# Kernel tuning notes

Hardware: AMD Instinct MI355X
Metric: run time of the kernel (lower is better)

Reference implementation:

```python
import jax, jax.numpy as jnp
import numpy as np

EPS = 1e-5


def conv3x3(x, w):
    # x: [B,C,H,W], w: [O,I,3,3], stride 1, pad 1 (torch Conv2d bias=False)
    return jax.lax.conv_general_dilated(
        x, w, window_strides=(1, 1), padding=((1, 1), (1, 1)),
        dimension_numbers=("NCHW", "OIHW", "NCHW"))


def batchnorm(y, g, b, m, v):
    # inference-style BN with running stats
    s = (g * jax.lax.rsqrt(v + EPS)).reshape(1, -1, 1, 1)
    t = (b - m * g * jax.lax.rsqrt(v + EPS)).reshape(1, -1, 1, 1)
    return y * s + t


def setup_inputs() -> dict:
    key = jax.random.key(0)
    ks = jax.random.split(key, 12)
    bs, c, h, w, T = 32, 64, 96, 96, 64
    inp = {}
    inp["x"] = jax.random.normal(ks[0], (bs, c, h, w), jnp.float32)
    inp["ref_x"] = jax.random.normal(ks[1], (bs, c, 1, 1), jnp.float32)
    inp["ref_types"] = jax.random.randint(ks[2], (bs,), 0, T, jnp.int32)
    # feat_extract: two BasicConv2d (conv3x3 no bias + BN + ReLU)
    inp["conv1_w"] = jax.random.normal(ks[3], (c, c, 3, 3), jnp.float32) * 0.05
    inp["bn1_g"] = jnp.ones((c,), jnp.float32)
    inp["bn1_b"] = jnp.zeros((c,), jnp.float32)
    inp["bn1_m"] = jnp.zeros((c,), jnp.float32)
    inp["bn1_v"] = jnp.ones((c,), jnp.float32)
    inp["conv2_w"] = jax.random.normal(ks[4], (c, c, 3, 3), jnp.float32) * 0.05
    inp["bn2_g"] = jnp.ones((c,), jnp.float32)
    inp["bn2_b"] = jnp.zeros((c,), jnp.float32)
    inp["bn2_m"] = jnp.zeros((c,), jnp.float32)
    inp["bn2_v"] = jnp.ones((c,), jnp.float32)
    # weight_mlp: Linear(c, 2c) -> ReLU -> Linear(2c, T)
    inp["mlp_w1"] = jax.random.normal(ks[5], (c, 2 * c), jnp.float32) * 0.05
    inp["mlp_b1"] = jnp.zeros((2 * c,), jnp.float32)
    inp["mlp_w2"] = jax.random.normal(ks[6], (2 * c, T), jnp.float32) * 0.05
    inp["mlp_b2"] = jnp.zeros((T,), jnp.float32)
    # reference buffer (torch registers zeros; use small randn so output is nontrivial)
    inp["ref_proj"] = jax.random.normal(ks[7], (T, c), jnp.float32) * 0.05
    return inp


def reference(x, ref_x, ref_types, conv1_w, bn1_g, bn1_b, bn1_m, bn1_v,
              conv2_w, bn2_g, bn2_b, bn2_m, bn2_v,
              mlp_w1, mlp_b1, mlp_w2, mlp_b2, ref_proj):
    momentum = jnp.float32(0.99)
    temperature = jnp.float32(1.0)
    bs, c, h, w = x.shape
    T = ref_proj.shape[0]

    # feat_extract + global average pool
    f = jax.nn.relu(batchnorm(conv3x3(x, conv1_w), bn1_g, bn1_b, bn1_m, bn1_v))
    f = jax.nn.relu(batchnorm(conv3x3(f, conv2_w), bn2_g, bn2_b, bn2_m, bn2_v))
    x_feat = f.mean(axis=(2, 3))  # [bs, c]

    # weight MLP -> tempered softmax
    type_logits = jax.nn.relu(x_feat @ mlp_w1 + mlp_b1) @ mlp_w2 + mlp_b2  # [bs, T]
    type_weights = jax.nn.softmax(type_logits / temperature, axis=1)

    # sequential per-sample EMA scatter, vectorized in closed form:
    # ref_new[t] = m^{k_t} * ref_proj[t] + sum_i 1[type_i=t] (1-m) m^{#later occ of t} v_i
    ref_vec = ref_x.reshape(bs, c)
    onehot = jax.nn.one_hot(ref_types, T, dtype=x.dtype)        # [bs, T]
    counts = onehot.sum(axis=0)                                  # [T]
    occ_after = counts[None, :] - jnp.cumsum(onehot, axis=0)     # strictly-after count
    w_i = (1.0 - momentum) * (momentum ** occ_after) * onehot    # [bs, T]
    ref_new = (momentum ** counts)[:, None] * ref_proj + w_i.T @ ref_vec  # [T, c]

    # weighted reference from (updated) buffer
    weighted_ref = (type_weights @ ref_new).reshape(bs, c, 1, 1)
    out = weighted_ref + ref_x

    # supervision loss: cross entropy (mean)
    logp = jax.nn.log_softmax(type_logits, axis=1)
    loss = -jnp.take_along_axis(logp, ref_types[:, None].astype(jnp.int32), axis=1).mean()
    return out, loss, ref_new
```

## Files before the change

kernel.cpp:

```cpp
#include <hip/hip_runtime.h>
#include <math.h>

#define BATCH 32
#define CH    64
#define HH    96
#define WW    96
#define NT    64

using short8 = __attribute__((ext_vector_type(8))) short;
using f32x16 = __attribute__((ext_vector_type(16))) float;

#define WS_XFS   0
#define WS_ZERO  8192
#define WS_A1    8448
#define WS_A2    82176
#define WS_XT    155904
#define WS_F1T   37904640
#define PLANE    9437184

__device__ __forceinline__ unsigned short b16(float f) {
    unsigned int u = __builtin_bit_cast(unsigned int, f);
    unsigned int r = (u + 0x7FFFu + ((u >> 16) & 1u)) >> 16;
    return (unsigned short)r;
}

__device__ __forceinline__ void gl_lds16(const void* g, void* l) {
    __builtin_amdgcn_global_load_lds(
        (const __attribute__((address_space(1))) unsigned int*)g,
        (__attribute__((address_space(3))) unsigned int*)l, 16, 0, 0);
}

__global__ void prep_small(const float* __restrict__ c1w, const float* __restrict__ c2w,
                           char* __restrict__ ws) {
    const int bid = blockIdx.x, tx = threadIdx.x;
    if (bid < 288) {
        const float* w = bid < 144 ? c1w : c2w;
        unsigned short* At = (unsigned short*)(ws + (bid < 144 ? WS_A1 : WS_A2));
        int idx = (bid % 144) * 256 + tx;
        int j = idx & 7, g1 = idx >> 3;
        int ga = g1 % 576, mc = g1 / 576;
        int c = mc & 3, mt = mc >> 2;
        int tap = ga >> 6, kb = (ga >> 5) & 1, ol = ga & 31;
        int o = mt * 32 + ol, ci = c * 16 + kb * 8 + j;
        At[idx] = b16(w[(o * 64 + ci) * 9 + tap]);
    } else {
        int i = (bid - 288) * 256 + tx;
        if (i < 2112) ((float*)ws)[i] = 0.f;
    }
}

__global__ __launch_bounds__(256)
void prep_x(const float* __restrict__ x, char* __restrict__ xt) {
    int gid = blockIdx.x * 256 + threadIdx.x;
    int cig = gid / 147456;
    int pp  = gid % 147456;
    int p   = pp * 2;
    int b   = p / 9216;
    int hw  = p % 9216;
    const float* src = x + (size_t)(b * 64 + cig * 8) * 9216 + hw;
    float2 v0 = *(const float2*)(src + 0 * 9216);
    float2 v1 = *(const float2*)(src + 1 * 9216);
    float2 v2 = *(const float2*)(src + 2 * 9216);
    float2 v3 = *(const float2*)(src + 3 * 9216);
    float2 v4 = *(const float2*)(src + 4 * 9216);
    float2 v5 = *(const float2*)(src + 5 * 9216);
    float2 v6 = *(const float2*)(src + 6 * 9216);
    float2 v7 = *(const float2*)(src + 7 * 9216);
    int c = cig >> 1, kb2 = cig & 1;
    char* dst = xt + (size_t)c * PLANE + (size_t)p * 32 + kb2 * 16;
    ushort4 a0, a1, c0, c1;
    a0.x = b16(v0.x); a0.y = b16(v1.x); a0.z = b16(v2.x); a0.w = b16(v3.x);
    a1.x = b16(v4.x); a1.y = b16(v5.x); a1.z = b16(v6.x); a1.w = b16(v7.x);
    c0.x = b16(v0.y); c0.y = b16(v1.y); c0.z = b16(v2.y); c0.w = b16(v3.y);
    c1.x = b16(v4.y); c1.y = b16(v5.y); c1.z = b16(v6.y); c1.w = b16(v7.y);
    *(ushort4*)(dst)      = a0; *(ushort4*)(dst + 8)  = a1;
    *(ushort4*)(dst + 32) = c0; *(ushort4*)(dst + 40) = c1;
}

template <int POOL>
__global__ __launch_bounds__(512, 2)
void conv_mfma(const char* __restrict__ xt, const char* __restrict__ Aprep,
               const char* __restrict__ zerop,
               const float* __restrict__ gg, const float* __restrict__ bb,
               const float* __restrict__ mm, const float* __restrict__ vv_,
               char* __restrict__ f1t, float* __restrict__ xfs) {
    __shared__ char smem[31232];
    float* s_s = (float*)(smem + 30720);
    float* s_t = s_s + 64;

    const int tx = threadIdx.x;
    const int r0 = blockIdx.x * 8;
    const int b  = blockIdx.y;
    const int wv = tx >> 6, l = tx & 63;
    const int rh = wv;
    const int kb = l >> 5, ln = l & 31;

    if (tx < 64) {
        float inv = rsqrtf(vv_[tx] + 1e-5f);
        s_s[tx] = gg[tx] * inv;
        s_t[tx] = bb[tx] - mm[tx] * gg[tx] * inv;
    }

    const char* sin[4];
    bool oob[4];
#pragma unroll
    for (int i = 0; i < 4; ++i) {
        int q = wv + 8 * i;
        int g = q * 64 + l;
        int row = g / 192, t = g % 192;
        int kb2 = t / 96, col = t % 96;
        int grow = r0 - 1 + row;
        oob[i] = (grow < 0) || (grow >= 96);
        int gr = oob[i] ? 0 : grow;
        sin[i] = xt + (size_t)((b * 96 + gr) * 96 + col) * 32 + kb2 * 16;
    }
    const char* abase = Aprep + (kb * 32 + ln) * 16;

    int bcol[3][3];
#pragma unroll
    for (int nt = 0; nt < 3; ++nt)
#pragma unroll
        for (int dw = 0; dw < 3; ++dw) {
            int cc = nt * 32 + ln + dw - 1;
            int ccc = cc < 0 ? 0 : (cc > 95 ? 95 : cc);
            bcol[nt][dw] = kb * 1536 + ccc * 16;
        }
    const bool msk0 = (ln == 0), msk2 = (ln == 31);

    f32x16 acc[2][3] = {};

#pragma unroll
    for (int c = 0; c < 4; ++c) {
        __syncthreads();
#pragma unroll
        for (int i = 0; i < 4; ++i) {
            int q = wv + 8 * i;
            if (q < 30) {
                const char* s = oob[i] ? zerop : (sin[i] + (size_t)c * PLANE);
                gl_lds16(s, smem + q * 1024);
            }
        }
        short8 af[2][9];
#pragma unroll
        for (int mt = 0; mt < 2; ++mt)
#pragma unroll
            for (int tap = 0; tap < 9; ++tap)
                af[mt][tap] = *(const short8*)(abase + mt * 36864 + c * 9216 + tap * 1024);
        __syncthreads();

        const char* brow = smem + rh * 3072;
#pragma unroll
        for (int tap = 0; tap < 9; ++tap) {
            const int dh = tap / 3, dw = tap % 3;
#pragma unroll
            for (int nt = 0; nt < 3; ++nt) {
                short8 bf = *(const short8*)(brow + dh * 3072 + bcol[nt][dw]);
                if (nt == 0 && dw == 0) bf = msk0 ? (short8){} : bf;
                if (nt == 2 && dw == 2) bf = msk2 ? (short8){} : bf;
                acc[0][nt] = __builtin_amdgcn_mfma_f32_32x32x16_bf16(af[0][tap], bf, acc[0][nt], 0, 0, 0);
                acc[1][nt] = __builtin_amdgcn_mfma_f32_32x32x16_bf16(af[1][tap], bf, acc[1][nt], 0, 0, 0);
            }
        }
    }

    const int r = r0 + rh;
    if (POOL == 0) {
#pragma unroll
        for (int nt = 0; nt < 3; ++nt) {
            int p = (b * 96 + r) * 96 + nt * 32 + ln;
            char* pb = f1t + (size_t)p * 32 + kb * 8;
#pragma unroll
            for (int mt = 0; mt < 2; ++mt)
#pragma unroll
                for (int qh = 0; qh < 4; ++qh) {
                    const int ob = mt * 32 + 8 * qh + 4 * kb;
                    float y0 = fmaxf(fmaf(acc[mt][nt][qh * 4 + 0], s_s[ob + 0], s_t[ob + 0]), 0.f);
                    float y1 = fmaxf(fmaf(acc[mt][nt][qh * 4 + 1], s_s[ob + 1], s_t[ob + 1]), 0.f);
                    float y2 = fmaxf(fmaf(acc[mt][nt][qh * 4 + 2], s_s[ob + 2], s_t[ob + 2]), 0.f);
                    float y3 = fmaxf(fmaf(acc[mt][nt][qh * 4 + 3], s_s[ob + 3], s_t[ob + 3]), 0.f);
                    uint2 pk;
                    pk.x = (unsigned)b16(y0) | ((unsigned)b16(y1) << 16);
                    pk.y = (unsigned)b16(y2) | ((unsigned)b16(y3) << 16);
                    *(uint2*)(pb + (size_t)(mt * 2 + (qh >> 1)) * PLANE + (qh & 1) * 16) = pk;
                }
        }
    } else {
#pragma unroll
        for (int mt = 0; mt < 2; ++mt)
#pragma unroll
            for (int qh = 0; qh < 4; ++qh)
#pragma unroll
                for (int j = 0; j < 4; ++j) {
                    const int o = mt * 32 + 8 * qh + 4 * kb + j;
                    const float ss = s_s[o], tt = s_t[o];
                    float y = fmaxf(fmaf(acc[mt][0][qh * 4 + j], ss, tt), 0.f)
                            + fmaxf(fmaf(acc[mt][1][qh * 4 + j], ss, tt), 0.f)
                            + fmaxf(fmaf(acc[mt][2][qh * 4 + j], ss, tt), 0.f);
#pragma unroll
                    for (int off = 1; off < 32; off <<= 1) y += __shfl_xor(y, off, 64);
                    if (ln == 0) atomicAdd(&xfs[b * 64 + o], y);
                }
    }
}

__global__ __launch_bounds__(1024)
void head_kernel(const float* __restrict__ xfs, const float* __restrict__ rx,
                 const int* __restrict__ ty_g,
                 const float* __restrict__ w1, const float* __restrict__ b1,
                 const float* __restrict__ w2, const float* __restrict__ b2,
                 const float* __restrict__ rproj, float* __restrict__ out) {
    __shared__ float xf[BATCH][64];
    __shared__ float hb[BATCH][128];
    __shared__ float lg[BATCH][NT];
    __shared__ float rnew[NT][64];
    __shared__ float rxs[BATCH * 64];
    __shared__ int   ty[BATCH];
    __shared__ float lossb[BATCH];

    const int tx = threadIdx.x;

    for (int i = tx; i < BATCH * 64; i += 1024) {
        xf[i >> 6][i & 63] = xfs[i] * (1.f / 9216.f);
        rxs[i] = rx[i];
    }
    if (tx < BATCH) ty[tx] = ty_g[tx];
    __syncthreads();

    {
        int idx = tx;
#pragma unroll
        for (int u = 0; u < 4; ++u, idx += 1024) {
            int bb_ = idx >> 7, j = idx & 127;
            float s = b1[j];
#pragma unroll 8
            for (int c = 0; c < 64; ++c) s = fmaf(xf[bb_][c], w1[c * 128 + j], s);
            hb[bb_][j] = fmaxf(s, 0.f);
        }
    }
    __syncthreads();

    {
        int idx = tx;
#pragma unroll
        for (int u = 0; u < 2; ++u, idx += 1024) {
            int bb_ = idx >> 6, t = idx & 63;
            float s = b2[t];
#pragma unroll 8
            for (int j = 0; j < 128; ++j) s = fmaf(hb[bb_][j], w2[j * 64 + t], s);
            lg[bb_][t] = s;
        }
    }
    __syncthreads();

    float (*tw)[NT] = (float (*)[NT])xf;
    if (tx < BATCH) {
        int b = tx;
        float mx = -1e30f;
        for (int t = 0; t < NT; ++t) mx = fmaxf(mx, lg[b][t]);
        float sum = 0.f;
        for (int t = 0; t < NT; ++t) sum += expf(lg[b][t] - mx);
        float inv = 1.f / sum;
        for (int t = 0; t < NT; ++t) tw[b][t] = expf(lg[b][t] - mx) * inv;
        lossb[b] = -(lg[b][ty[b]] - mx - logf(sum));
    }
    __syncthreads();

    for (int idx = tx; idx < NT * 64; idx += 1024) {
        int t = idx >> 6, c = idx & 63;
        float r = rproj[idx];
#pragma unroll 8
        for (int i = 0; i < BATCH; ++i)
            if (ty[i] == t) r = 0.99f * r + 0.01f * rxs[i * 64 + c];
        rnew[t][c] = r;
        out[2049 + idx] = r;
    }
    __syncthreads();

    for (int idx = tx; idx < BATCH * 64; idx += 1024) {
        int b = idx >> 6, c = idx & 63;
        float s = 0.f;
#pragma unroll 8
        for (int t = 0; t < NT; ++t) s = fmaf(tw[b][t], rnew[t][c], s);
        out[idx] = s + rxs[idx];
    }
    if (tx == 0) {
        float s = 0.f;
        for (int b = 0; b < BATCH; ++b) s += lossb[b];
        out[2048] = s * (1.f / 32.f);
    }
}

extern "C" void kernel_launch(void* const* d_in, const int* in_sizes, int n_in,
                              void* d_out, int out_size, void* d_ws, size_t ws_size,
                              hipStream_t stream) {
    const float* x    = (const float*)d_in[0];
    const float* rx   = (const float*)d_in[1];
    const int*   ty   = (const int*)d_in[2];
    const float* c1w  = (const float*)d_in[3];
    const float* bn1g = (const float*)d_in[4];
    const float* bn1b = (const float*)d_in[5];
    const float* bn1m = (const float*)d_in[6];
    const float* bn1v = (const float*)d_in[7];
    const float* c2w  = (const float*)d_in[8];
    const float* bn2g = (const float*)d_in[9];
    const float* bn2b = (const float*)d_in[10];
    const float* bn2m = (const float*)d_in[11];
    const float* bn2v = (const float*)d_in[12];
    const float* w1   = (const float*)d_in[13];
    const float* b1   = (const float*)d_in[14];
    const float* w2   = (const float*)d_in[15];
    const float* b2   = (const float*)d_in[16];
    const float* rpj  = (const float*)d_in[17];

    char* ws = (char*)d_ws;
    float* xfs = (float*)(ws + WS_XFS);
    char*  zp  = ws + WS_ZERO;
    char*  A1  = ws + WS_A1;
    char*  A2  = ws + WS_A2;
    char*  x_t = ws + WS_XT;
    char*  f1t = ws + WS_F1T;
    float* out = (float*)d_out;

    prep_small<<<297, 256, 0, stream>>>(c1w, c2w, ws);
    prep_x<<<4608, 256, 0, stream>>>(x, x_t);

    dim3 grid(12, 32);
    conv_mfma<0><<<grid, 512, 0, stream>>>(x_t, A1, zp, bn1g, bn1b, bn1m, bn1v, f1t, nullptr);
    conv_mfma<1><<<grid, 512, 0, stream>>>(f1t, A2, zp, bn2g, bn2b, bn2m, bn2v, nullptr, xfs);

    head_kernel<<<1, 1024, 0, stream>>>(xfs, rx, ty, w1, b1, w2, b2, rpj, out);
}
```

Baseline: 305.2 us.

## Double-buffer conv input tiles in LDS and stage weights via LDS with smaller blocks

The conv kernel now uses 256-thread blocks covering 4 output rows (grid doubled to 24x32) instead of 512 threads over 8 rows. Input channel-chunk tiles are double-buffered in LDS, so the next chunk's global-to-LDS loads are issued before the current chunk's MFMAs. Weight fragments are also staged into LDS per chunk rather than loaded into registers, which needed a matching reorder of the weight prep layout. This aims to hide load latency and cut register pressure, at the cost of more LDS per block (about 55 KB), extra halo re-reads from the smaller row tiles, and an added barrier pair per chunk for the weight reload.

```diff
diff --git a/kernel.cpp b/kernel.cpp
--- a/kernel.cpp
+++ b/kernel.cpp
@@ -17,6 +17,7 @@
 #define WS_XT    155904
 #define WS_F1T   37904640
 #define PLANE    9437184
+#define ACHUNK   18432
 
 __device__ __forceinline__ unsigned short b16(float f) {
     unsigned int u = __builtin_bit_cast(unsigned int, f);
@@ -37,10 +38,11 @@
         const float* w = bid < 144 ? c1w : c2w;
         unsigned short* At = (unsigned short*)(ws + (bid < 144 ? WS_A1 : WS_A2));
         int idx = (bid % 144) * 256 + tx;
-        int j = idx & 7, g1 = idx >> 3;
-        int ga = g1 % 576, mc = g1 / 576;
-        int c = mc & 3, mt = mc >> 2;
-        int tap = ga >> 6, kb = (ga >> 5) & 1, ol = ga & 31;
+        int j = idx & 7, ga_g = idx >> 3;
+        int c = ga_g / 1152, gc = ga_g % 1152;
+        int mtt = gc >> 6, kbol = gc & 63;
+        int mt = mtt / 9, tap = mtt % 9;
+        int kb = kbol >> 5, ol = kbol & 31;
         int o = mt * 32 + ol, ci = c * 16 + kb * 8 + j;
         At[idx] = b16(w[(o * 64 + ci) * 9 + tap]);
     } else {
@@ -78,18 +80,18 @@
 }
 
 template <int POOL>
-__global__ __launch_bounds__(512, 2)
+__global__ __launch_bounds__(256, 2)
 void conv_mfma(const char* __restrict__ xt, const char* __restrict__ Aprep,
                const char* __restrict__ zerop,
                const float* __restrict__ gg, const float* __restrict__ bb,
                const float* __restrict__ mm, const float* __restrict__ vv_,
                char* __restrict__ f1t, float* __restrict__ xfs) {
-    __shared__ char smem[31232];
-    float* s_s = (float*)(smem + 30720);
+    __shared__ char smem[55808];
+    float* s_s = (float*)(smem + 55296);
     float* s_t = s_s + 64;
 
     const int tx = threadIdx.x;
-    const int r0 = blockIdx.x * 8;
+    const int r0 = blockIdx.x * 4;
     const int b  = blockIdx.y;
     const int wv = tx >> 6, l = tx & 63;
     const int rh = wv;
@@ -101,65 +103,85 @@
         s_t[tx] = bb[tx] - mm[tx] * gg[tx] * inv;
     }
 
-    const char* sin[4];
-    bool oob[4];
-#pragma unroll
-    for (int i = 0; i < 4; ++i) {
-        int q = wv + 8 * i;
-        int g = q * 64 + l;
+    const char* isrc[5];
+    bool ioob[5];
+#pragma unroll
+    for (int i = 0; i < 5; ++i) {
+        int g = i * 256 + tx;
         int row = g / 192, t = g % 192;
         int kb2 = t / 96, col = t % 96;
         int grow = r0 - 1 + row;
-        oob[i] = (grow < 0) || (grow >= 96);
-        int gr = oob[i] ? 0 : grow;
-        sin[i] = xt + (size_t)((b * 96 + gr) * 96 + col) * 32 + kb2 * 16;
-    }
-    const char* abase = Aprep + (kb * 32 + ln) * 16;
-
-    int bcol[3][3];
+        ioob[i] = (grow < 0) || (grow >= 96) || (g >= 1152);
+        int gr = (grow < 0 || grow >= 96) ? 0 : grow;
+        isrc[i] = xt + (size_t)((b * 96 + gr) * 96 + col) * 32 + kb2 * 16;
+    }
+    const char* abase = Aprep + (size_t)tx * 16;
+
+    int colpart[3][3];
 #pragma unroll
     for (int nt = 0; nt < 3; ++nt)
 #pragma unroll
         for (int dw = 0; dw < 3; ++dw) {
             int cc = nt * 32 + ln + dw - 1;
             int ccc = cc < 0 ? 0 : (cc > 95 ? 95 : cc);
-            bcol[nt][dw] = kb * 1536 + ccc * 16;
+            colpart[nt][dw] = kb * 1536 + ccc * 16;
         }
     const bool msk0 = (ln == 0), msk2 = (ln == 31);
 
+    auto stage_input = [&](int c, int sel) {
+#pragma unroll
+        for (int i = 0; i < 5; ++i) {
+            int g = i * 256 + tx;
+            if (g < 1152) {
+                const char* s = ioob[i] ? zerop : (isrc[i] + (size_t)c * PLANE);
+                gl_lds16(s, smem + sel * 18432 + (size_t)g * 16);
+            }
+        }
+    };
+    auto stage_a = [&](int c) {
+#pragma unroll
+        for (int i = 0; i < 5; ++i) {
+            int g = i * 256 + tx;
+            if (g < 1152)
+                gl_lds16(abase + (size_t)c * ACHUNK + i * 4096, smem + 36864 + (size_t)g * 16);
+        }
+    };
+
     f32x16 acc[2][3] = {};
 
+    stage_input(0, 0);
+    stage_a(0);
+    asm volatile("s_waitcnt vmcnt(0)");
+    __syncthreads();
+
 #pragma unroll
     for (int c = 0; c < 4; ++c) {
-        __syncthreads();
-#pragma unroll
-        for (int i = 0; i < 4; ++i) {
-            int q = wv + 8 * i;
-            if (q < 30) {
-                const char* s = oob[i] ? zerop : (sin[i] + (size_t)c * PLANE);
-                gl_lds16(s, smem + q * 1024);
-            }
-        }
-        short8 af[2][9];
-#pragma unroll
-        for (int mt = 0; mt < 2; ++mt)
-#pragma unroll
-            for (int tap = 0; tap < 9; ++tap)
-                af[mt][tap] = *(const short8*)(abase + mt * 36864 + c * 9216 + tap * 1024);
-        __syncthreads();
-
-        const char* brow = smem + rh * 3072;
+        const int cur = c & 1;
+        if (c < 3) stage_input(c + 1, cur ^ 1);
+
+        const char* ib = smem + cur * 18432;
 #pragma unroll
         for (int tap = 0; tap < 9; ++tap) {
             const int dh = tap / 3, dw = tap % 3;
+            short8 a0 = *(const short8*)(smem + 36864 + (tap)     * 1024 + kb * 512 + ln * 16);
+            short8 a1 = *(const short8*)(smem + 36864 + (9 + tap) * 1024 + kb * 512 + ln * 16);
+            const char* brow = ib + (rh + dh) * 3072;
 #pragma unroll
             for (int nt = 0; nt < 3; ++nt) {
-                short8 bf = *(const short8*)(brow + dh * 3072 + bcol[nt][dw]);
+                short8 bf = *(const short8*)(brow + colpart[nt][dw]);
                 if (nt == 0 && dw == 0) bf = msk0 ? (short8){} : bf;
                 if (nt == 2 && dw == 2) bf = msk2 ? (short8){} : bf;
-                acc[0][nt] = __builtin_amdgcn_mfma_f32_32x32x16_bf16(af[0][tap], bf, acc[0][nt], 0, 0, 0);
-                acc[1][nt] = __builtin_amdgcn_mfma_f32_32x32x16_bf16(af[1][tap], bf, acc[1][nt], 0, 0, 0);
+                acc[0][nt] = __builtin_amdgcn_mfma_f32_32x32x16_bf16(a0, bf, acc[0][nt], 0, 0, 0);
+                acc[1][nt] = __builtin_amdgcn_mfma_f32_32x32x16_bf16(a1, bf, acc[1][nt], 0, 0, 0);
             }
+        }
+
+        if (c < 3) {
+            asm volatile("s_waitcnt vmcnt(0)");
+            __syncthreads();
+            stage_a(c + 1);
+            asm volatile("s_waitcnt vmcnt(0)");
+            __syncthreads();
         }
     }
 
@@ -324,9 +346,9 @@
     prep_small<<<297, 256, 0, stream>>>(c1w, c2w, ws);
     prep_x<<<4608, 256, 0, stream>>>(x, x_t);
 
-    dim3 grid(12, 32);
-    conv_mfma<0><<<grid, 512, 0, stream>>>(x_t, A1, zp, bn1g, bn1b, bn1m, bn1v, f1t, nullptr);
-    conv_mfma<1><<<grid, 512, 0, stream>>>(f1t, A2, zp, bn2g, bn2b, bn2m, bn2v, nullptr, xfs);
+    dim3 grid(24, 32);
+    conv_mfma<0><<<grid, 256, 0, stream>>>(x_t, A1, zp, bn1g, bn1b, bn1m, bn1v, f1t, nullptr);
+    conv_mfma<1><<<grid, 256, 0, stream>>>(f1t, A2, zp, bn2g, bn2b, bn2m, bn2v, nullptr, xfs);
 
     head_kernel<<<1, 1024, 0, stream>>>(xfs, rx, ty, w1, b1, w2, b2, rpj, out);
 }
```

Measured after the change: 288.6 us. 1.06x faster.
